# Optimization experiments

Hardware: AMD Instinct MI355X
Metric: run time of the kernel (lower is better)

The kernel has to match this reference:

```python
import jax, jax.numpy as jnp
import numpy as np
from math import factorial

MAX_L = 3

def _l_list(max_l):
    ls = []
    for L in range(max_l + 1):
        for lx in range(L, -1, -1):
            for ly in range(L - lx, -1, -1):
                ls.append((lx, ly, L - lx - ly))
    return ls

def _multinom(v):
    return factorial(sum(v)) // (factorial(v[0]) * factorial(v[1]) * factorial(v[2]))

def _compositions(m):
    # all (ax, ay, az) >= 0 with ax+ay+az == m
    return [(ax, ay, m - ax - ay) for ax in range(m + 1) for ay in range(m + 1 - ax)]

def _build_sym_tensors(max_l):
    ls = _l_list(max_l)
    idx = {l: i for i, l in enumerate(ls)}
    n_l = len(ls)
    # nu=2 invariants: one per degree L = 1..max_l:  sum_{|l|=L} multinom(l) * A_l * A_l
    S2 = np.zeros((n_l, n_l, max_l), dtype=np.float32)
    for l in ls:
        L = sum(l)
        if L >= 1:
            S2[idx[l], idx[l], L - 1] = _multinom(l)
    # nu=3 invariants: (r1.r2)^m12 (r1.r3)^m13 (r2.r3)^m23 with each vector degree >= 1
    keys = []
    for m12 in range(max_l + 1):
        for m13 in range(max_l + 1 - m12):
            for m23 in range(max_l + 1):
                if (m12 + m23 <= max_l and m13 + m23 <= max_l
                        and m12 + m13 >= 1 and m12 + m23 >= 1 and m13 + m23 >= 1):
                    keys.append((m12, m13, m23))
    S3 = np.zeros((n_l, n_l, n_l, len(keys)), dtype=np.float32)
    for a, (m12, m13, m23) in enumerate(keys):
        for va in _compositions(m12):
            for vb in _compositions(m13):
                for vc in _compositions(m23):
                    l1 = (va[0] + vb[0], va[1] + vb[1], va[2] + vb[2])
                    l2 = (va[0] + vc[0], va[1] + vc[1], va[2] + vc[2])
                    l3 = (vb[0] + vc[0], vb[1] + vc[1], vb[2] + vc[2])
                    p = float(_multinom(va) * _multinom(vb) * _multinom(vc))
                    S3[idx[l1], idx[l2], idx[l3], a] += p
    return jnp.asarray(S2), jnp.asarray(S3)

def setup_inputs() -> dict:
    key = jax.random.key(0)
    N, R, C = 2048, 4, 16
    n_l = len(_l_list(MAX_L))  # 20
    node_attr = jax.random.normal(key, (N, R, n_l, C), dtype=jnp.float32)
    S2, S3 = _build_sym_tensors(MAX_L)  # [20,20,3], [20,20,20,13]
    return {"node_attr": node_attr, "S2": S2, "S3": S3}

def reference(node_attr, S2, S3):
    # node_attr: [N, R, n_l, C]; output: [N, R, 1 + a2 + a3, C]
    out0 = node_attr[:, :, :1, :]                                   # nu=1 term (l=(0,0,0))
    pair = jnp.einsum('ijlk,ijmk->ijlmk', node_attr, node_attr)     # [N,R,n_l,n_l,C]
    out2 = jnp.einsum('ijlmk,lma->ijak', pair, S2)                  # [N,R,a2,C]
    # nu=3 without materializing the [N,R,n_l,n_l,n_l,C] outer product:
    tmp = jnp.einsum('ijlmk,lmna->ijnak', pair, S3)                 # [N,R,n_l,a3,C]
    out3 = jnp.einsum('ijnak,ijnk->ijak', tmp, node_attr)           # [N,R,a3,C]
    return jnp.concatenate([out0, out2, out3], axis=2)
```

## Files before the change

kernel.cpp:

```cpp
#include <hip/hip_runtime.h>
#include <utility>
#include <cstddef>

constexpr int MAXL = 3;
constexpr int NL   = 20;
constexpr int NA2  = MAXL;
constexpr int NA3  = 13;
constexpr int NOUT = 1 + NA2 + NA3;
constexpr int C    = 16;

constexpr long long fact_(int n){ long long r=1; for(int i=2;i<=n;i++) r*=i; return r; }
constexpr float multinom_(int x,int y,int z){
    return (float)(fact_(x+y+z)/(fact_(x)*fact_(y)*fact_(z)));
}
constexpr int lidx_(int x,int y,int z){
    int i=0;
    for(int L=0;L<=MAXL;L++)
      for(int lx=L;lx>=0;lx--)
        for(int ly=L-lx;ly>=0;ly--){
          int lz=L-lx-ly;
          if(lx==x&&ly==y&&lz==z) return i;
          i++;
        }
    return -1;
}

struct S3Pat { int n; int l1[400]; int l2[400]; int l3[400]; int a[400]; float v[400]; };
constexpr S3Pat build_s3_(){
    S3Pat p{};
    int a=0;
    for(int m12=0;m12<=MAXL;m12++)
    for(int m13=0;m13<=MAXL-m12;m13++)
    for(int m23=0;m23<=MAXL;m23++){
        if(m12+m23>MAXL||m13+m23>MAXL) continue;
        if(m12+m13<1||m12+m23<1||m13+m23<1) continue;
        for(int ax=0;ax<=m12;ax++)for(int ay=0;ay<=m12-ax;ay++)
        for(int bx=0;bx<=m13;bx++)for(int by=0;by<=m13-bx;by++)
        for(int cx=0;cx<=m23;cx++)for(int cy=0;cy<=m23-cx;cy++){
            int az=m12-ax-ay, bz=m13-bx-by, cz=m23-cx-cy;
            int i1=lidx_(ax+bx,ay+by,az+bz);
            int i2=lidx_(ax+cx,ay+cy,az+cz);
            int i3=lidx_(bx+cx,by+cy,bz+cz);
            float pv=multinom_(ax,ay,az)*multinom_(bx,by,bz)*multinom_(cx,cy,cz);
            bool found=false;
            for(int t=0;t<p.n;t++){
                if(p.l1[t]==i1&&p.l2[t]==i2&&p.l3[t]==i3&&p.a[t]==a){
                    p.v[t]+=pv; found=true; break;
                }
            }
            if(!found){ p.l1[p.n]=i1;p.l2[p.n]=i2;p.l3[p.n]=i3;p.a[p.n]=a;p.v[p.n]=pv;p.n++; }
        }
        a++;
    }
    return p;
}
constexpr S3Pat S3P = build_s3_();

struct S2Pat { int n; int l[NL]; int a[NL]; float v[NL]; };
constexpr S2Pat build_s2_(){
    S2Pat p{};
    int i=0;
    for(int L=0;L<=MAXL;L++)
      for(int lx=L;lx>=0;lx--)
        for(int ly=L-lx;ly>=0;ly--){
            int lz=L-lx-ly;
            if(L>=1){ p.l[p.n]=i; p.a[p.n]=L-1; p.v[p.n]=multinom_(lx,ly,lz); p.n++; }
            i++;
        }
    return p;
}
constexpr S2Pat S2P = build_s2_();

template<size_t... E>
__device__ __forceinline__ void s2_accum_(const float* x, float* o, std::index_sequence<E...>){
    ((o[1 + S2P.a[E]] = fmaf(S2P.v[E] * x[S2P.l[E]], x[S2P.l[E]], o[1 + S2P.a[E]])), ...);
}
template<size_t... E>
__device__ __forceinline__ void s3_accum_(const float* x, float* o, std::index_sequence<E...>){
    ((o[1 + NA2 + S3P.a[E]] =
        fmaf(S3P.v[E] * x[S3P.l1[E]], x[S3P.l2[E]] * x[S3P.l3[E]], o[1 + NA2 + S3P.a[E]])), ...);
}

constexpr int TQ      = 16;
constexpr int IN_ROW  = NL * C;
constexpr int IN_PAD  = 328;
constexpr int OUT_ROW = NOUT * C;
constexpr int OUT_PAD = 280;

__global__ __launch_bounds__(256) void sym_kernel(const float* __restrict__ na,
                                                  float* __restrict__ out){
    __shared__ float sin_[TQ][IN_PAD];
    __shared__ float sout_[TQ][OUT_PAD];
    const int tid = threadIdx.x;
    const size_t q0 = (size_t)blockIdx.x * TQ;

    const float4* gin = (const float4*)(na + q0 * IN_ROW);
    #pragma unroll
    for (int j = 0; j < 5; ++j) {
        int i = tid + j * 256;
        int r = i / 80;
        int c = (i - r * 80) * 4;
        float4 v = gin[i];
        *(float4*)&sin_[r][c] = v;
    }
    __syncthreads();

    const int r = tid >> 4;
    const int k = tid & 15;
    float x[NL];
    #pragma unroll
    for (int l = 0; l < NL; ++l) x[l] = sin_[r][k + l * 16];

    float o[NOUT];
    #pragma unroll
    for (int i = 0; i < NOUT; ++i) o[i] = 0.0f;
    o[0] = x[0];
    s2_accum_(x, o, std::make_index_sequence<S2P.n>{});
    s3_accum_(x, o, std::make_index_sequence<S3P.n>{});

    #pragma unroll
    for (int a = 0; a < NOUT; ++a) sout_[r][k + a * 16] = o[a];
    __syncthreads();

    float4* gout = (float4*)(out + q0 * OUT_ROW);
    #pragma unroll
    for (int j = 0; j < 5; ++j) {
        int i = tid + j * 256;
        if (i < 1088) {
            int rr = i / 68;
            int cc = (i - rr * 68) * 4;
            gout[i] = *(float4*)&sout_[rr][cc];
        }
    }
}

extern "C" void kernel_launch(void* const* d_in, const int* in_sizes, int n_in,
                              void* d_out, int out_size, void* d_ws, size_t ws_size,
                              hipStream_t stream) {
    const float* na = (const float*)d_in[0];
    float* out = (float*)d_out;
    int nq = in_sizes[0] / (NL * C);
    int blocks = nq / TQ;
    sym_kernel<<<blocks, 256, 0, stream>>>(na, out);
}
```

Before: 10.52 us.

## Split S3 term evaluation across two half-blocks and write outputs directly

Halves the rows per block (TQ 16 to 8) and splits each row's work between two groups of 128 threads. A compile-time search picks the output index where the FMA counts of the two halves are closest, so each half computes a balanced share of S2/S3 terms. The shared-memory output staging and its second barrier are removed; each thread writes its outputs straight to global memory as strided 64-byte segments across 16 lanes. This doubles the block count and shortens each thread's serial chain, at the cost of loading the input twice per row and giving up float4 coalesced stores.

```diff
diff --git a/kernel.cpp b/kernel.cpp
--- a/kernel.cpp
+++ b/kernel.cpp
@@ -71,42 +71,60 @@
 }
 constexpr S2Pat S2P = build_s2_();
 
+struct Split { int key; int term; };
+constexpr Split find_split_(){
+    Split best{0,0}; long bestd = 1L<<40;
+    for (int key=0; key<=NA3; ++key){
+        int t=0;
+        for (int i=0;i<S3P.n;i++) if (S3P.a[i] < key) t++;
+        long h0 = 2L*S2P.n + 3L*t;
+        long h1 = 3L*(S3P.n - t);
+        long d = h0>h1 ? h0-h1 : h1-h0;
+        if (d < bestd){ bestd=d; best.key=key; best.term=t; }
+    }
+    return best;
+}
+constexpr Split SPL = find_split_();
+
 template<size_t... E>
 __device__ __forceinline__ void s2_accum_(const float* x, float* o, std::index_sequence<E...>){
     ((o[1 + S2P.a[E]] = fmaf(S2P.v[E] * x[S2P.l[E]], x[S2P.l[E]], o[1 + S2P.a[E]])), ...);
 }
-template<size_t... E>
-__device__ __forceinline__ void s3_accum_(const float* x, float* o, std::index_sequence<E...>){
-    ((o[1 + NA2 + S3P.a[E]] =
-        fmaf(S3P.v[E] * x[S3P.l1[E]], x[S3P.l2[E]] * x[S3P.l3[E]], o[1 + NA2 + S3P.a[E]])), ...);
+template<size_t OFF, size_t... E>
+__device__ __forceinline__ void s3_range_(const float* x, float* o, std::index_sequence<E...>){
+    ((o[1 + NA2 + S3P.a[OFF + E]] =
+        fmaf(S3P.v[OFF + E] * x[S3P.l1[OFF + E]],
+             x[S3P.l2[OFF + E]] * x[S3P.l3[OFF + E]],
+             o[1 + NA2 + S3P.a[OFF + E]])), ...);
 }
 
-constexpr int TQ      = 16;
+constexpr int TQ      = 8;
 constexpr int IN_ROW  = NL * C;
 constexpr int IN_PAD  = 328;
 constexpr int OUT_ROW = NOUT * C;
-constexpr int OUT_PAD = 280;
 
 __global__ __launch_bounds__(256) void sym_kernel(const float* __restrict__ na,
                                                   float* __restrict__ out){
     __shared__ float sin_[TQ][IN_PAD];
-    __shared__ float sout_[TQ][OUT_PAD];
     const int tid = threadIdx.x;
     const size_t q0 = (size_t)blockIdx.x * TQ;
 
     const float4* gin = (const float4*)(na + q0 * IN_ROW);
     #pragma unroll
-    for (int j = 0; j < 5; ++j) {
+    for (int j = 0; j < 3; ++j) {
         int i = tid + j * 256;
-        int r = i / 80;
-        int c = (i - r * 80) * 4;
-        float4 v = gin[i];
-        *(float4*)&sin_[r][c] = v;
+        if (i < 640) {
+            int r = i / 80;
+            int c = (i - r * 80) * 4;
+            *(float4*)&sin_[r][c] = gin[i];
+        }
     }
     __syncthreads();
 
-    const int r = tid >> 4;
+    const int h = tid >> 7;
+    const int r = (tid >> 4) & 7;
     const int k = tid & 15;
+
     float x[NL];
     #pragma unroll
     for (int l = 0; l < NL; ++l) x[l] = sin_[r][k + l * 16];
@@ -114,23 +132,18 @@
     float o[NOUT];
     #pragma unroll
     for (int i = 0; i < NOUT; ++i) o[i] = 0.0f;
-    o[0] = x[0];
-    s2_accum_(x, o, std::make_index_sequence<S2P.n>{});
-    s3_accum_(x, o, std::make_index_sequence<S3P.n>{});
 
-    #pragma unroll
-    for (int a = 0; a < NOUT; ++a) sout_[r][k + a * 16] = o[a];
-    __syncthreads();
-
-    float4* gout = (float4*)(out + q0 * OUT_ROW);
-    #pragma unroll
-    for (int j = 0; j < 5; ++j) {
-        int i = tid + j * 256;
-        if (i < 1088) {
-            int rr = i / 68;
-            int cc = (i - rr * 68) * 4;
-            gout[i] = *(float4*)&sout_[rr][cc];
-        }
+    float* ob = out + (q0 + r) * OUT_ROW + k;
+    if (h == 0) {
+        o[0] = x[0];
+        s2_accum_(x, o, std::make_index_sequence<S2P.n>{});
+        s3_range_<0>(x, o, std::make_index_sequence<SPL.term>{});
+        #pragma unroll
+        for (int a = 0; a < 1 + NA2 + SPL.key; ++a) ob[a * C] = o[a];
+    } else {
+        s3_range_<SPL.term>(x, o, std::make_index_sequence<S3P.n - SPL.term>{});
+        #pragma unroll
+        for (int a = 1 + NA2 + SPL.key; a < NOUT; ++a) ob[a * C] = o[a];
     }
 }
 
```

Result: no change. 10.46 us (-0.6%).
